# Kernel tuning notes

Hardware: AMD Instinct MI355X
Metric: run time of the kernel (lower is better)

The kernel has to match this reference:

```python
import jax, jax.numpy as jnp
import numpy as np

N_HEAD = 16

def setup_inputs() -> dict:
    key = jax.random.key(0)
    k1, k2, k3 = jax.random.split(key, 3)
    B, T, C = 4, 2048, 2048
    x = jax.random.normal(k1, (B, T, C), dtype=jnp.float32)
    # nn.Linear weights stored as [out, in]; we keep [in, out] for x @ W
    Wqkv = jax.random.normal(k2, (C, 3 * C), dtype=jnp.float32) * (1.0 / np.sqrt(C))
    Wproj = jax.random.normal(k3, (C, C), dtype=jnp.float32) * (1.0 / np.sqrt(C))
    return {"x": x, "Wqkv": Wqkv, "Wproj": Wproj}

def reference(x, Wqkv, Wproj):
    B, T, C = x.shape
    H = N_HEAD
    hd = C // H
    qkv = x @ Wqkv                                  # [B,T,3C]
    qkv = qkv.reshape(B, T, 3, H, hd)
    q = qkv[:, :, 0].transpose(0, 2, 1, 3)          # [B,H,T,hd]
    k = qkv[:, :, 1].transpose(0, 2, 1, 3)
    v = qkv[:, :, 2].transpose(0, 2, 1, 3)
    scale = 1.0 / np.sqrt(hd).astype(np.float32)
    scores = jnp.einsum('bhqd,bhkd->bhqk', q, k) * scale
    causal = jnp.tril(jnp.ones((T, T), dtype=bool))
    scores = jnp.where(causal, scores, jnp.finfo(scores.dtype).min)
    attn = jax.nn.softmax(scores, axis=-1)
    y = jnp.einsum('bhqk,bhkd->bhqd', attn, v)      # [B,H,T,hd]
    y = y.transpose(0, 2, 1, 3).reshape(B, T, C)
    return y @ Wproj  # dropout is identity in eval / p=0
```

## Files before the change

kernel.cpp:

```cpp
#include <hip/hip_runtime.h>
#include <hip/hip_bf16.h>
#include <cstdint>

typedef __bf16 bf16;
typedef __bf16 bf16x8 __attribute__((ext_vector_type(8)));
typedef float f32x4 __attribute__((ext_vector_type(4)));
typedef float f32x8 __attribute__((ext_vector_type(8)));
typedef uint32_t u32x4 __attribute__((ext_vector_type(4)));

constexpr int Bz = 4, T = 2048, Cdim = 2048, NH = 16, HD = 128;
constexpr int QKVC = 3 * Cdim;
constexpr int QKC = 2 * Cdim;
constexpr float NEG_BIG = -3.0e4f;

__device__ __forceinline__ void load_lds16(const bf16* g, const bf16* l) {
  __builtin_amdgcn_global_load_lds(
      (const __attribute__((address_space(1))) void*)g,
      (__attribute__((address_space(3))) void*)l, 16, 0, 0);
}

__device__ __forceinline__ uint32_t pack2bf(float lo, float hi) {
  uint16_t a = __builtin_bit_cast(uint16_t, (bf16)lo);
  uint16_t b = __builtin_bit_cast(uint16_t, (bf16)hi);
  return ((uint32_t)b << 16) | (uint32_t)a;
}

__global__ __launch_bounds__(256)
void cvt_bf16_k(const float* __restrict__ in, bf16* __restrict__ out) {
  size_t i = (size_t)blockIdx.x * 256 + threadIdx.x;
  f32x8 v = *(const f32x8*)(in + i * 8);
  bf16x8 h;
#pragma unroll
  for (int j = 0; j < 8; ++j) h[j] = (bf16)v[j];
  *(bf16x8*)(out + i * 8) = h;
}

__global__ __launch_bounds__(256)
void transpose_cvt_k(const float* __restrict__ in, bf16* __restrict__ out,
                     int R, int Ccols) {
  __shared__ bf16 tile[32][33];
  int c0 = blockIdx.x * 32, r0 = blockIdx.y * 32;
  int tx = threadIdx.x, ty = threadIdx.y;
#pragma unroll
  for (int i = 0; i < 4; ++i)
    tile[ty + i * 8][tx] = (bf16)in[(size_t)(r0 + ty + i * 8) * Ccols + c0 + tx];
  __syncthreads();
#pragma unroll
  for (int i = 0; i < 4; ++i)
    out[(size_t)(c0 + ty + i * 8) * R + r0 + tx] = tile[tx][ty + i * 8];
}

template <bool CF32, bool SCATV>
__global__ __launch_bounds__(512, 2)
void gemm256_k(const bf16* __restrict__ A, const bf16* __restrict__ BT,
               void* __restrict__ Craw, bf16* __restrict__ Vt,
               int M, int N, int K, int ldc) {
  extern __shared__ bf16 lds[];
  const int nK = K >> 6;

  const int nbx = gridDim.x;
  const int nwg = nbx * gridDim.y;
  const int orig = blockIdx.x + blockIdx.y * nbx;
  const int q8 = nwg >> 3;
  const int wgid = (orig & 7) * q8 + (orig >> 3);
  const size_t col0 = (size_t)(wgid % nbx) * 256;
  const size_t row0 = (size_t)(wgid / nbx) * 256;

  const int tid = threadIdx.x;
  const int w = tid >> 6, lane = tid & 63;
  const int qn = lane & 15, quad = lane >> 4;
  const int wm = w >> 2, wn = w & 3;

  const int rl8 = lane >> 3;
  const int scol = ((lane & 7) ^ rl8) << 3;
  const size_t gOff = (size_t)(w * 8 + rl8) * K + scol;
  const int ldsW = w * 512;

  const int csA0 = (quad * 8) ^ ((qn & 7) << 3);
  const int csA1 = (32 + quad * 8) ^ ((qn & 7) << 3);
  const int aBaseIdx = wm * 8192 + qn * 64;
  const int bBaseIdx = 16384 + (wn >> 1) * 8192 + ((wn & 1) * 64 + qn) * 64;

  f32x4 acc[8][4];
  f32x4 zero4 = {0.f, 0.f, 0.f, 0.f};
#pragma unroll
  for (int m = 0; m < 8; ++m)
#pragma unroll
    for (int n = 0; n < 4; ++n) acc[m][n] = zero4;

  auto stageA = [&](int c, int h, int t) {
    const bf16* g = A + (row0 + h * 128) * (size_t)K + (size_t)t * 64 + gOff;
    const bf16* l = lds + c * 32768 + h * 8192 + ldsW;
    load_lds16(g, l);
    load_lds16(g + (size_t)64 * K, l + 4096);
  };
  auto stageB = [&](int c, int h, int t) {
    const bf16* g = BT + (col0 + h * 128) * (size_t)K + (size_t)t * 64 + gOff;
    const bf16* l = lds + c * 32768 + 16384 + h * 8192 + ldsW;
    load_lds16(g, l);
    load_lds16(g + (size_t)64 * K, l + 4096);
  };

  stageA(0, 0, 0); stageA(0, 1, 0);
  stageB(0, 0, 0); stageB(0, 1, 0);
  if (nK > 1) { stageB(1, 0, 1); stageB(1, 1, 1); }
  asm volatile("s_waitcnt vmcnt(4)" ::: "memory");
  asm volatile("s_barrier" ::: "memory");

  for (int t = 0; t < nK; ++t) {
    const int c = t & 1, cn = c ^ 1;
    const int cE = c * 32768;

    bf16x8 a0[4][2], b0[2][2], b1[2][2];
#pragma unroll
    for (int m = 0; m < 4; ++m) {
      a0[m][0] = *(const bf16x8*)&lds[cE + aBaseIdx + m * 1024 + csA0];
      a0[m][1] = *(const bf16x8*)&lds[cE + aBaseIdx + m * 1024 + csA1];
    }
#pragma unroll
    for (int n = 0; n < 2; ++n) {
      b0[n][0] = *(const bf16x8*)&lds[cE + bBaseIdx + n * 1024 + csA0];
      b0[n][1] = *(const bf16x8*)&lds[cE + bBaseIdx + n * 1024 + csA1];
      b1[n][0] = *(const bf16x8*)&lds[cE + bBaseIdx + (n + 2) * 1024 + csA0];
      b1[n][1] = *(const bf16x8*)&lds[cE + bBaseIdx + (n + 2) * 1024 + csA1];
    }
    if (t + 1 < nK) stageA(cn, 1, t + 1);
    __builtin_amdgcn_s_setprio(1);
#pragma unroll
    for (int m = 0; m < 4; ++m)
#pragma unroll
      for (int n = 0; n < 2; ++n) {
        acc[m][n] = __builtin_amdgcn_mfma_f32_16x16x32_bf16(a0[m][0], b0[n][0], acc[m][n], 0, 0, 0);
        acc[m][n] = __builtin_amdgcn_mfma_f32_16x16x32_bf16(a0[m][1], b0[n][1], acc[m][n], 0, 0, 0);
      }
    __builtin_amdgcn_s_setprio(0);
    asm volatile("s_barrier" ::: "memory");

    if (t + 1 < nK) stageA(cn, 0, t + 1);
    __builtin_amdgcn_s_setprio(1);
#pragma unroll
    for (int m = 0; m < 4; ++m)
#pragma unroll
      for (int n = 0; n < 2; ++n) {
        acc[m][n + 2] = __builtin_amdgcn_mfma_f32_16x16x32_bf16(a0[m][0], b1[n][0], acc[m][n + 2], 0, 0, 0);
        acc[m][n + 2] = __builtin_amdgcn_mfma_f32_16x16x32_bf16(a0[m][1], b1[n][1], acc[m][n + 2], 0, 0, 0);
      }
    __builtin_amdgcn_s_setprio(0);
    asm volatile("s_barrier" ::: "memory");

    bf16x8 a1[4][2];
#pragma unroll
    for (int m = 0; m < 4; ++m) {
      a1[m][0] = *(const bf16x8*)&lds[cE + aBaseIdx + (m + 4) * 1024 + csA0];
      a1[m][1] = *(const bf16x8*)&lds[cE + aBaseIdx + (m + 4) * 1024 + csA1];
    }
    if (t + 2 < nK) stageB(c, 0, t + 2);
    __builtin_amdgcn_s_setprio(1);
#pragma unroll
    for (int m = 0; m < 4; ++m)
#pragma unroll
      for (int n = 0; n < 2; ++n) {
        acc[m + 4][n] = __builtin_amdgcn_mfma_f32_16x16x32_bf16(a1[m][0], b0[n][0], acc[m + 4][n], 0, 0, 0);
        acc[m + 4][n] = __builtin_amdgcn_mfma_f32_16x16x32_bf16(a1[m][1], b0[n][1], acc[m + 4][n], 0, 0, 0);
      }
    __builtin_amdgcn_s_setprio(0);
    asm volatile("s_barrier" ::: "memory");

    if (t + 2 < nK) {
      stageB(c, 1, t + 2);
      asm volatile("s_waitcnt vmcnt(4)" ::: "memory");
    } else {
      asm volatile("s_waitcnt vmcnt(0)" ::: "memory");
    }
    __builtin_amdgcn_s_setprio(1);
#pragma unroll
    for (int m = 0; m < 4; ++m)
#pragma unroll
      for (int n = 0; n < 2; ++n) {
        acc[m + 4][n + 2] = __builtin_amdgcn_mfma_f32_16x16x32_bf16(a1[m][0], b1[n][0], acc[m + 4][n + 2], 0, 0, 0);
        acc[m + 4][n + 2] = __builtin_amdgcn_mfma_f32_16x16x32_bf16(a1[m][1], b1[n][1], acc[m + 4][n + 2], 0, 0, 0);
      }
    __builtin_amdgcn_s_setprio(0);
    asm volatile("s_barrier" ::: "memory");
  }

  if (SCATV && (int)col0 >= QKC) {
#pragma unroll
    for (int m = 0; m < 8; ++m)
#pragma unroll
      for (int n = 0; n < 4; ++n)
#pragma unroll
        for (int rr = 0; rr < 4; ++rr) {
          int row = (int)row0 + wm * 128 + m * 16 + quad * 4 + rr;
          int bb = row >> 11, tt = row & (T - 1);
          int cv = (int)col0 + wn * 64 + n * 16 + qn - QKC;
          int hh = cv >> 7, d = cv & 127;
          Vt[((size_t)(bb * NH + hh) * HD + d) * T + tt] = (bf16)acc[m][n][rr];
        }
  } else {
#pragma unroll
    for (int m = 0; m < 8; ++m)
#pragma unroll
      for (int n = 0; n < 4; ++n)
#pragma unroll
        for (int rr = 0; rr < 4; ++rr) {
          size_t idx = (row0 + wm * 128 + m * 16 + quad * 4 + rr) * (size_t)ldc +
                       col0 + wn * 64 + n * 16 + qn;
          if (CF32) ((float*)Craw)[idx] = acc[m][n][rr];
          else      ((bf16*)Craw)[idx] = (bf16)acc[m][n][rr];
        }
  }
}

constexpr int KSTR = 136, VSTR = 72;

__global__ __launch_bounds__(512, 4)
void attn_k(const bf16* __restrict__ qk, const bf16* __restrict__ vt,
            bf16* __restrict__ y) {
  const int b = blockIdx.z, h = blockIdx.y;
  const int qb = (int)(gridDim.x - 1 - blockIdx.x);
  const int qt0 = qb * 128;
  const int tid = threadIdx.x;
  const int w = tid >> 6, lane = tid & 63;
  const int qn = lane & 15, quad = lane >> 4;
  const int q0 = qt0 + w * 16;

  __shared__ __align__(16) bf16 Ks[64 * KSTR];
  __shared__ __align__(16) bf16 Vs[128 * VSTR];

  const bf16* qkB = qk + (size_t)b * T * QKC + h * HD;
  const bf16* vtB = vt + (size_t)(b * NH + h) * HD * T;
  const bf16* kBase = qkB + Cdim;

  bf16x8 qF[4];
  {
    const float scale = 0.088388347648318447f;
    const bf16* qRow = qkB + (size_t)(q0 + qn) * QKC;
#pragma unroll
    for (int c = 0; c < 4; ++c) {
      bf16x8 v = *(const bf16x8*)(qRow + c * 32 + quad * 8);
#pragma unroll
      for (int j = 0; j < 8; ++j) v[j] = (bf16)((float)v[j] * scale);
      qF[c] = v;
    }
  }

  float m_i = NEG_BIG, l_i = 0.f;
  f32x4 zero4 = {0.f, 0.f, 0.f, 0.f};
  f32x4 o[8];
#pragma unroll
  for (int cc = 0; cc < 8; ++cc) o[cc] = zero4;

  const int kr  = tid >> 4;
  const int kc8 = (tid & 15) << 3;
  const int vd  = tid >> 3;
  const int vk8 = (tid & 7) << 3;

  const int addrA = ((lane & 15) + ((quad & 1) << 5)) << 2;
  const int addrB = addrA + 64;

  const int nT = 2 * qb + 2;

  bf16x8 rK0 = *(const bf16x8*)(kBase + (size_t)kr * QKC + kc8);
  bf16x8 rK1 = *(const bf16x8*)(kBase + (size_t)(kr + 32) * QKC + kc8);
  bf16x8 rV0 = *(const bf16x8*)(vtB + (size_t)vd * T + vk8);
  bf16x8 rV1 = *(const bf16x8*)(vtB + (size_t)(vd + 64) * T + vk8);

  for (int t = 0; t < nT; ++t) {
    const int kt0 = t * 64;
    __syncthreads();
    *(bf16x8*)&Ks[kr * KSTR + kc8] = rK0;
    *(bf16x8*)&Ks[(kr + 32) * KSTR + kc8] = rK1;
    *(bf16x8*)&Vs[vd * VSTR + vk8] = rV0;
    *(bf16x8*)&Vs[(vd + 64) * VSTR + vk8] = rV1;
    __syncthreads();
    if (t + 1 < nT) {
      const int kn = kt0 + 64;
      rK0 = *(const bf16x8*)(kBase + (size_t)(kn + kr) * QKC + kc8);
      rK1 = *(const bf16x8*)(kBase + (size_t)(kn + kr + 32) * QKC + kc8);
      rV0 = *(const bf16x8*)(vtB + (size_t)vd * T + kn + vk8);
      rV1 = *(const bf16x8*)(vtB + (size_t)(vd + 64) * T + kn + vk8);
    }
    if (kt0 > q0 + 15) continue;

    f32x4 s[4] = {zero4, zero4, zero4, zero4};
    __builtin_amdgcn_s_setprio(1);
#pragma unroll
    for (int c = 0; c < 4; ++c)
#pragma unroll
      for (int ks = 0; ks < 4; ++ks) {
        bf16x8 kf = *(const bf16x8*)&Ks[(ks * 16 + qn) * KSTR + c * 32 + quad * 8];
        s[ks] = __builtin_amdgcn_mfma_f32_16x16x32_bf16(kf, qF[c], s[ks], 0, 0, 0);
      }
    __builtin_amdgcn_s_setprio(0);

    if (kt0 + 63 > q0) {
      const int qv = q0 + qn;
#pragma unroll
      for (int ks = 0; ks < 4; ++ks)
#pragma unroll
        for (int rr = 0; rr < 4; ++rr)
          if (kt0 + ks * 16 + quad * 4 + rr > qv) s[ks][rr] = NEG_BIG;
    }

    float mx = s[0][0];
#pragma unroll
    for (int ks = 0; ks < 4; ++ks)
#pragma unroll
      for (int rr = 0; rr < 4; ++rr) mx = fmaxf(mx, s[ks][rr]);
    mx = fmaxf(mx, __shfl_xor(mx, 16));
    mx = fmaxf(mx, __shfl_xor(mx, 32));

    if (!__all(mx - m_i <= 8.0f)) {
      float mn = fmaxf(m_i, mx);
      float alpha = __expf(m_i - mn);
      m_i = mn;
      l_i *= alpha;
      float aR[4];
#pragma unroll
      for (int rr = 0; rr < 4; ++rr) aR[rr] = __shfl(alpha, quad * 4 + rr);
#pragma unroll
      for (int cc = 0; cc < 8; ++cc)
#pragma unroll
        for (int rr = 0; rr < 4; ++rr) o[cc][rr] *= aR[rr];
    }

    float rs = 0.f;
#pragma unroll
    for (int ks = 0; ks < 4; ++ks)
#pragma unroll
      for (int rr = 0; rr < 4; ++rr) {
        float pv = __expf(s[ks][rr] - m_i);
        s[ks][rr] = pv;
        rs += pv;
      }
    rs += __shfl_xor(rs, 16);
    rs += __shfl_xor(rs, 32);
    l_i += rs;

    uint32_t pku[4][2];
#pragma unroll
    for (int ks = 0; ks < 4; ++ks)
#pragma unroll
      for (int b2 = 0; b2 < 2; ++b2)
        pku[ks][b2] = pack2bf(s[ks][2 * b2], s[ks][2 * b2 + 1]);

    const int hi2 = quad >> 1;
    __builtin_amdgcn_s_setprio(1);
#pragma unroll
    for (int c = 0; c < 2; ++c) {
      uint32_t lo0A = (uint32_t)__builtin_amdgcn_ds_bpermute(addrA, (int)pku[2 * c][0]);
      uint32_t lo1A = (uint32_t)__builtin_amdgcn_ds_bpermute(addrA, (int)pku[2 * c][1]);
      uint32_t lo0B = (uint32_t)__builtin_amdgcn_ds_bpermute(addrB, (int)pku[2 * c][0]);
      uint32_t lo1B = (uint32_t)__builtin_amdgcn_ds_bpermute(addrB, (int)pku[2 * c][1]);
      uint32_t hi0A = (uint32_t)__builtin_amdgcn_ds_bpermute(addrA, (int)pku[2 * c + 1][0]);
      uint32_t hi1A = (uint32_t)__builtin_amdgcn_ds_bpermute(addrA, (int)pku[2 * c + 1][1]);
      uint32_t hi0B = (uint32_t)__builtin_amdgcn_ds_bpermute(addrB, (int)pku[2 * c + 1][0]);
      uint32_t hi1B = (uint32_t)__builtin_amdgcn_ds_bpermute(addrB, (int)pku[2 * c + 1][1]);
      u32x4 pw;
      pw[0] = hi2 ? hi0A : lo0A;
      pw[1] = hi2 ? hi1A : lo1A;
      pw[2] = hi2 ? hi0B : lo0B;
      pw[3] = hi2 ? hi1B : lo1B;
      bf16x8 pF = __builtin_bit_cast(bf16x8, pw);
#pragma unroll
      for (int cc = 0; cc < 8; ++cc) {
        bf16x8 vf = *(const bf16x8*)&Vs[(cc * 16 + qn) * VSTR + c * 32 + quad * 8];
        o[cc] = __builtin_amdgcn_mfma_f32_16x16x32_bf16(pF, vf, o[cc], 0, 0, 0);
      }
    }
    __builtin_amdgcn_s_setprio(0);
  }

  float linv[4];
#pragma unroll
  for (int rr = 0; rr < 4; ++rr) {
    float lr = __shfl(l_i, quad * 4 + rr);
    linv[rr] = 1.f / fmaxf(lr, 1e-30f);
  }
  bf16* yB = y + (size_t)b * T * Cdim + h * HD;
#pragma unroll
  for (int cc = 0; cc < 8; ++cc)
#pragma unroll
    for (int rr = 0; rr < 4; ++rr)
      yB[(size_t)(q0 + quad * 4 + rr) * Cdim + cc * 16 + qn] =
          (bf16)(o[cc][rr] * linv[rr]);
}

extern "C" void kernel_launch(void* const* d_in, const int* in_sizes, int n_in,
                              void* d_out, int out_size, void* d_ws, size_t ws_size,
                              hipStream_t stream) {
  const float* x     = (const float*)d_in[0];
  const float* Wqkv  = (const float*)d_in[1];
  const float* Wproj = (const float*)d_in[2];
  float* out = (float*)d_out;

  char* ws = (char*)d_ws;
  bf16* qkbuf  = (bf16*)(ws);
  bf16* Vt     = (bf16*)(ws + (size_t)64 * 1024 * 1024);
  bf16* WqkvT  = (bf16*)(ws + (size_t)96 * 1024 * 1024);
  bf16* y      = WqkvT;
  bf16* WprojT = (bf16*)(ws + (size_t)128 * 1024 * 1024);
  bf16* xb     = (bf16*)d_out;

  cvt_bf16_k<<<dim3((Bz * T * Cdim) / (256 * 8)), 256, 0, stream>>>(x, xb);
  transpose_cvt_k<<<dim3(QKVC / 32, Cdim / 32), dim3(32, 8), 0, stream>>>(
      Wqkv, WqkvT, Cdim, QKVC);
  transpose_cvt_k<<<dim3(Cdim / 32, Cdim / 32), dim3(32, 8), 0, stream>>>(
      Wproj, WprojT, Cdim, Cdim);

  gemm256_k<false, true><<<dim3(QKVC / 256, (Bz * T) / 256), 512, 131072, stream>>>(
      xb, WqkvT, (void*)qkbuf, Vt, Bz * T, QKVC, Cdim, QKC);

  attn_k<<<dim3(T / 128, NH, Bz), 512, 0, stream>>>(qkbuf, Vt, y);

  gemm256_k<true, false><<<dim3(Cdim / 256, (Bz * T) / 256), 512, 131072, stream>>>(
      y, WprojT, (void*)out, nullptr, Bz * T, Cdim, Cdim, Cdim);
}
```

Before: 603.8 us.

## Pair complementary causal query tiles per attention block to balance work

Each attention block now handles two 128-row query tiles, qb and 15-qb. The two tiles share every K/V tile loaded into shared memory, and every block gets an equal amount of causal work, which removes the triangular load imbalance and halves the K/V traffic for the short tile. The grid shrinks to half the blocks, and launch bounds drop from 4 to 2 blocks per CU to allow the doubled accumulator and Q registers. Occupancy falls and the per-iteration register pressure rises.

```diff
diff --git a/kernel.cpp b/kernel.cpp
--- a/kernel.cpp
+++ b/kernel.cpp
@@ -214,16 +214,17 @@
 
 constexpr int KSTR = 136, VSTR = 72;
 
-__global__ __launch_bounds__(512, 4)
+__global__ __launch_bounds__(512, 2)
 void attn_k(const bf16* __restrict__ qk, const bf16* __restrict__ vt,
             bf16* __restrict__ y) {
   const int b = blockIdx.z, h = blockIdx.y;
-  const int qb = (int)(gridDim.x - 1 - blockIdx.x);
-  const int qt0 = qb * 128;
+  const int qbA = blockIdx.x;
+  const int qbB = 15 - qbA;
   const int tid = threadIdx.x;
   const int w = tid >> 6, lane = tid & 63;
   const int qn = lane & 15, quad = lane >> 4;
-  const int q0 = qt0 + w * 16;
+  const int q0A = qbA * 128 + w * 16;
+  const int q0B = qbB * 128 + w * 16;
 
   __shared__ __align__(16) bf16 Ks[64 * KSTR];
   __shared__ __align__(16) bf16 Vs[128 * VSTR];
@@ -232,24 +233,29 @@
   const bf16* vtB = vt + (size_t)(b * NH + h) * HD * T;
   const bf16* kBase = qkB + Cdim;
 
-  bf16x8 qF[4];
+  bf16x8 qFA[4], qFB[4];
   {
     const float scale = 0.088388347648318447f;
-    const bf16* qRow = qkB + (size_t)(q0 + qn) * QKC;
+    const bf16* qRowA = qkB + (size_t)(q0A + qn) * QKC;
+    const bf16* qRowB = qkB + (size_t)(q0B + qn) * QKC;
 #pragma unroll
     for (int c = 0; c < 4; ++c) {
-      bf16x8 v = *(const bf16x8*)(qRow + c * 32 + quad * 8);
-#pragma unroll
-      for (int j = 0; j < 8; ++j) v[j] = (bf16)((float)v[j] * scale);
-      qF[c] = v;
-    }
-  }
-
-  float m_i = NEG_BIG, l_i = 0.f;
+      bf16x8 va = *(const bf16x8*)(qRowA + c * 32 + quad * 8);
+      bf16x8 vb = *(const bf16x8*)(qRowB + c * 32 + quad * 8);
+#pragma unroll
+      for (int j = 0; j < 8; ++j) {
+        va[j] = (bf16)((float)va[j] * scale);
+        vb[j] = (bf16)((float)vb[j] * scale);
+      }
+      qFA[c] = va; qFB[c] = vb;
+    }
+  }
+
+  float mA = NEG_BIG, lA = 0.f, mB = NEG_BIG, lB = 0.f;
   f32x4 zero4 = {0.f, 0.f, 0.f, 0.f};
-  f32x4 o[8];
-#pragma unroll
-  for (int cc = 0; cc < 8; ++cc) o[cc] = zero4;
+  f32x4 oA[8], oB[8];
+#pragma unroll
+  for (int cc = 0; cc < 8; ++cc) { oA[cc] = zero4; oB[cc] = zero4; }
 
   const int kr  = tid >> 4;
   const int kc8 = (tid & 15) << 3;
@@ -258,8 +264,75 @@
 
   const int addrA = ((lane & 15) + ((quad & 1) << 5)) << 2;
   const int addrB = addrA + 64;
-
-  const int nT = 2 * qb + 2;
+  const int hi2 = quad >> 1;
+
+  auto softmax_pack = [&](f32x4 (&s)[4], int q0p, int kt0, float& m_i,
+                          float& l_i, f32x4 (&o)[8], uint32_t (&pku)[4][2]) {
+    if (kt0 + 63 > q0p) {
+      const int qv = q0p + qn;
+#pragma unroll
+      for (int ks = 0; ks < 4; ++ks)
+#pragma unroll
+        for (int rr = 0; rr < 4; ++rr)
+          if (kt0 + ks * 16 + quad * 4 + rr > qv) s[ks][rr] = NEG_BIG;
+    }
+    float mx = s[0][0];
+#pragma unroll
+    for (int ks = 0; ks < 4; ++ks)
+#pragma unroll
+      for (int rr = 0; rr < 4; ++rr) mx = fmaxf(mx, s[ks][rr]);
+    mx = fmaxf(mx, __shfl_xor(mx, 16));
+    mx = fmaxf(mx, __shfl_xor(mx, 32));
+    if (!__all(mx - m_i <= 8.0f)) {
+      float mn = fmaxf(m_i, mx);
+      float alpha = __expf(m_i - mn);
+      m_i = mn;
+      l_i *= alpha;
+      float aR[4];
+#pragma unroll
+      for (int rr = 0; rr < 4; ++rr) aR[rr] = __shfl(alpha, quad * 4 + rr);
+#pragma unroll
+      for (int cc = 0; cc < 8; ++cc)
+#pragma unroll
+        for (int rr = 0; rr < 4; ++rr) o[cc][rr] *= aR[rr];
+    }
+    float rs = 0.f;
+#pragma unroll
+    for (int ks = 0; ks < 4; ++ks)
+#pragma unroll
+      for (int rr = 0; rr < 4; ++rr) {
+        float pv = __expf(s[ks][rr] - m_i);
+        s[ks][rr] = pv;
+        rs += pv;
+      }
+    rs += __shfl_xor(rs, 16);
+    rs += __shfl_xor(rs, 32);
+    l_i += rs;
+#pragma unroll
+    for (int ks = 0; ks < 4; ++ks)
+#pragma unroll
+      for (int b2 = 0; b2 < 2; ++b2)
+        pku[ks][b2] = pack2bf(s[ks][2 * b2], s[ks][2 * b2 + 1]);
+  };
+
+  auto redist = [&](uint32_t (&pku)[4][2], int c) -> bf16x8 {
+    uint32_t lo0A = (uint32_t)__builtin_amdgcn_ds_bpermute(addrA, (int)pku[2 * c][0]);
+    uint32_t lo1A = (uint32_t)__builtin_amdgcn_ds_bpermute(addrA, (int)pku[2 * c][1]);
+    uint32_t lo0B = (uint32_t)__builtin_amdgcn_ds_bpermute(addrB, (int)pku[2 * c][0]);
+    uint32_t lo1B = (uint32_t)__builtin_amdgcn_ds_bpermute(addrB, (int)pku[2 * c][1]);
+    uint32_t hi0A = (uint32_t)__builtin_amdgcn_ds_bpermute(addrA, (int)pku[2 * c + 1][0]);
+    uint32_t hi1A = (uint32_t)__builtin_amdgcn_ds_bpermute(addrA, (int)pku[2 * c + 1][1]);
+    uint32_t hi0B = (uint32_t)__builtin_amdgcn_ds_bpermute(addrB, (int)pku[2 * c + 1][0]);
+    uint32_t hi1B = (uint32_t)__builtin_amdgcn_ds_bpermute(addrB, (int)pku[2 * c + 1][1]);
+    u32x4 pw;
+    pw[0] = hi2 ? hi0A : lo0A;
+    pw[1] = hi2 ? hi1A : lo1A;
+    pw[2] = hi2 ? hi0B : lo0B;
+    pw[3] = hi2 ? hi1B : lo1B;
+    return __builtin_bit_cast(bf16x8, pw);
+  };
+
+  const int nT = 2 * qbB + 2;
 
   bf16x8 rK0 = *(const bf16x8*)(kBase + (size_t)kr * QKC + kc8);
   bf16x8 rK1 = *(const bf16x8*)(kBase + (size_t)(kr + 32) * QKC + kc8);
@@ -281,110 +354,93 @@
       rV0 = *(const bf16x8*)(vtB + (size_t)vd * T + kn + vk8);
       rV1 = *(const bf16x8*)(vtB + (size_t)(vd + 64) * T + kn + vk8);
     }
-    if (kt0 > q0 + 15) continue;
-
-    f32x4 s[4] = {zero4, zero4, zero4, zero4};
-    __builtin_amdgcn_s_setprio(1);
-#pragma unroll
-    for (int c = 0; c < 4; ++c)
-#pragma unroll
-      for (int ks = 0; ks < 4; ++ks) {
-        bf16x8 kf = *(const bf16x8*)&Ks[(ks * 16 + qn) * KSTR + c * 32 + quad * 8];
-        s[ks] = __builtin_amdgcn_mfma_f32_16x16x32_bf16(kf, qF[c], s[ks], 0, 0, 0);
-      }
-    __builtin_amdgcn_s_setprio(0);
-
-    if (kt0 + 63 > q0) {
-      const int qv = q0 + qn;
-#pragma unroll
-      for (int ks = 0; ks < 4; ++ks)
-#pragma unroll
-        for (int rr = 0; rr < 4; ++rr)
-          if (kt0 + ks * 16 + quad * 4 + rr > qv) s[ks][rr] = NEG_BIG;
-    }
-
-    float mx = s[0][0];
-#pragma unroll
-    for (int ks = 0; ks < 4; ++ks)
-#pragma unroll
-      for (int rr = 0; rr < 4; ++rr) mx = fmaxf(mx, s[ks][rr]);
-    mx = fmaxf(mx, __shfl_xor(mx, 16));
-    mx = fmaxf(mx, __shfl_xor(mx, 32));
-
-    if (!__all(mx - m_i <= 8.0f)) {
-      float mn = fmaxf(m_i, mx);
-      float alpha = __expf(m_i - mn);
-      m_i = mn;
-      l_i *= alpha;
-      float aR[4];
-#pragma unroll
-      for (int rr = 0; rr < 4; ++rr) aR[rr] = __shfl(alpha, quad * 4 + rr);
-#pragma unroll
-      for (int cc = 0; cc < 8; ++cc)
-#pragma unroll
-        for (int rr = 0; rr < 4; ++rr) o[cc][rr] *= aR[rr];
-    }
-
-    float rs = 0.f;
-#pragma unroll
-    for (int ks = 0; ks < 4; ++ks)
-#pragma unroll
-      for (int rr = 0; rr < 4; ++rr) {
-        float pv = __expf(s[ks][rr] - m_i);
-        s[ks][rr] = pv;
-        rs += pv;
-      }
-    rs += __shfl_xor(rs, 16);
-    rs += __shfl_xor(rs, 32);
-    l_i += rs;
-
-    uint32_t pku[4][2];
-#pragma unroll
-    for (int ks = 0; ks < 4; ++ks)
-#pragma unroll
-      for (int b2 = 0; b2 < 2; ++b2)
-        pku[ks][b2] = pack2bf(s[ks][2 * b2], s[ks][2 * b2 + 1]);
-
-    const int hi2 = quad >> 1;
-    __builtin_amdgcn_s_setprio(1);
-#pragma unroll
-    for (int c = 0; c < 2; ++c) {
-      uint32_t lo0A = (uint32_t)__builtin_amdgcn_ds_bpermute(addrA, (int)pku[2 * c][0]);
-      uint32_t lo1A = (uint32_t)__builtin_amdgcn_ds_bpermute(addrA, (int)pku[2 * c][1]);
-      uint32_t lo0B = (uint32_t)__builtin_amdgcn_ds_bpermute(addrB, (int)pku[2 * c][0]);
-      uint32_t lo1B = (uint32_t)__builtin_amdgcn_ds_bpermute(addrB, (int)pku[2 * c][1]);
-      uint32_t hi0A = (uint32_t)__builtin_amdgcn_ds_bpermute(addrA, (int)pku[2 * c + 1][0]);
-      uint32_t hi1A = (uint32_t)__builtin_amdgcn_ds_bpermute(addrA, (int)pku[2 * c + 1][1]);
-      uint32_t hi0B = (uint32_t)__builtin_amdgcn_ds_bpermute(addrB, (int)pku[2 * c + 1][0]);
-      uint32_t hi1B = (uint32_t)__builtin_amdgcn_ds_bpermute(addrB, (int)pku[2 * c + 1][1]);
-      u32x4 pw;
-      pw[0] = hi2 ? hi0A : lo0A;
-      pw[1] = hi2 ? hi1A : lo1A;
-      pw[2] = hi2 ? hi0B : lo0B;
-      pw[3] = hi2 ? hi1B : lo1B;
-      bf16x8 pF = __builtin_bit_cast(bf16x8, pw);
-#pragma unroll
-      for (int cc = 0; cc < 8; ++cc) {
-        bf16x8 vf = *(const bf16x8*)&Vs[(cc * 16 + qn) * VSTR + c * 32 + quad * 8];
-        o[cc] = __builtin_amdgcn_mfma_f32_16x16x32_bf16(pF, vf, o[cc], 0, 0, 0);
-      }
-    }
-    __builtin_amdgcn_s_setprio(0);
-  }
-
-  float linv[4];
-#pragma unroll
-  for (int rr = 0; rr < 4; ++rr) {
-    float lr = __shfl(l_i, quad * 4 + rr);
-    linv[rr] = 1.f / fmaxf(lr, 1e-30f);
-  }
+    const bool actA = (kt0 <= q0A + 15);
+    const bool actB = (kt0 <= q0B + 15);
+    if (!actB) continue;
+
+    f32x4 sA[4] = {zero4, zero4, zero4, zero4};
+    f32x4 sB[4] = {zero4, zero4, zero4, zero4};
+    __builtin_amdgcn_s_setprio(1);
+    if (actA) {
+#pragma unroll
+      for (int c = 0; c < 4; ++c)
+#pragma unroll
+        for (int ks = 0; ks < 4; ++ks) {
+          bf16x8 kf = *(const bf16x8*)&Ks[(ks * 16 + qn) * KSTR + c * 32 + quad * 8];
+          sA[ks] = __builtin_amdgcn_mfma_f32_16x16x32_bf16(kf, qFA[c], sA[ks], 0, 0, 0);
+          sB[ks] = __builtin_amdgcn_mfma_f32_16x16x32_bf16(kf, qFB[c], sB[ks], 0, 0, 0);
+        }
+    } else {
+#pragma unroll
+      for (int c = 0; c < 4; ++c)
+#pragma unroll
+        for (int ks = 0; ks < 4; ++ks) {
+          bf16x8 kf = *(const bf16x8*)&Ks[(ks * 16 + qn) * KSTR + c * 32 + quad * 8];
+          sB[ks] = __builtin_amdgcn_mfma_f32_16x16x32_bf16(kf, qFB[c], sB[ks], 0, 0, 0);
+        }
+    }
+    __builtin_amdgcn_s_setprio(0);
+
+    uint32_t pkuA[4][2], pkuB[4][2];
+    if (actA) softmax_pack(sA, q0A, kt0, mA, lA, oA, pkuA);
+    softmax_pack(sB, q0B, kt0, mB, lB, oB, pkuB);
+
+    __builtin_amdgcn_s_setprio(1);
+    if (actA) {
+#pragma unroll
+      for (int c = 0; c < 2; ++c) {
+        bf16x8 pFA = redist(pkuA, c);
+        bf16x8 pFB = redist(pkuB, c);
+#pragma unroll
+        for (int cc = 0; cc < 8; ++cc) {
+          bf16x8 vf = *(const bf16x8*)&Vs[(cc * 16 + qn) * VSTR + c * 32 + quad * 8];
+          oA[cc] = __builtin_amdgcn_mfma_f32_16x16x32_bf16(pFA, vf, oA[cc], 0, 0, 0);
+          oB[cc] = __builtin_amdgcn_mfma_f32_16x16x32_bf16(pFB, vf, oB[cc], 0, 0, 0);
+        }
+      }
+    } else {
+#pragma unroll
+      for (int c = 0; c < 2; ++c) {
+        bf16x8 pFB = redist(pkuB, c);
+#pragma unroll
+        for (int cc = 0; cc < 8; ++cc) {
+          bf16x8 vf = *(const bf16x8*)&Vs[(cc * 16 + qn) * VSTR + c * 32 + quad * 8];
+          oB[cc] = __builtin_amdgcn_mfma_f32_16x16x32_bf16(pFB, vf, oB[cc], 0, 0, 0);
+        }
+      }
+    }
+    __builtin_amdgcn_s_setprio(0);
+  }
+
   bf16* yB = y + (size_t)b * T * Cdim + h * HD;
-#pragma unroll
-  for (int cc = 0; cc < 8; ++cc)
-#pragma unroll
-    for (int rr = 0; rr < 4; ++rr)
-      yB[(size_t)(q0 + quad * 4 + rr) * Cdim + cc * 16 + qn] =
-          (bf16)(o[cc][rr] * linv[rr]);
+  {
+    float linv[4];
+#pragma unroll
+    for (int rr = 0; rr < 4; ++rr) {
+      float lr = __shfl(lA, quad * 4 + rr);
+      linv[rr] = 1.f / fmaxf(lr, 1e-30f);
+    }
+#pragma unroll
+    for (int cc = 0; cc < 8; ++cc)
+#pragma unroll
+      for (int rr = 0; rr < 4; ++rr)
+        yB[(size_t)(q0A + quad * 4 + rr) * Cdim + cc * 16 + qn] =
+            (bf16)(oA[cc][rr] * linv[rr]);
+  }
+  {
+    float linv[4];
+#pragma unroll
+    for (int rr = 0; rr < 4; ++rr) {
+      float lr = __shfl(lB, quad * 4 + rr);
+      linv[rr] = 1.f / fmaxf(lr, 1e-30f);
+    }
+#pragma unroll
+    for (int cc = 0; cc < 8; ++cc)
+#pragma unroll
+      for (int rr = 0; rr < 4; ++rr)
+        yB[(size_t)(q0B + quad * 4 + rr) * Cdim + cc * 16 + qn] =
+            (bf16)(oB[cc][rr] * linv[rr]);
+  }
 }
 
 extern "C" void kernel_launch(void* const* d_in, const int* in_sizes, int n_in,
@@ -412,7 +468,7 @@
   gemm256_k<false, true><<<dim3(QKVC / 256, (Bz * T) / 256), 512, 131072, stream>>>(
       xb, WqkvT, (void*)qkbuf, Vt, Bz * T, QKVC, Cdim, QKC);
 
-  attn_k<<<dim3(T / 128, NH, Bz), 512, 0, stream>>>(qkbuf, Vt, y);
+  attn_k<<<dim3(T / 256, NH, Bz), 512, 0, stream>>>(qkbuf, Vt, y);
 
   gemm256_k<true, false><<<dim3(Cdim / 256, (Bz * T) / 256), 512, 131072, stream>>>(
       y, WprojT, (void*)out, nullptr, Bz * T, Cdim, Cdim, Cdim);
```

Result: faster. 550.3 us (-8.9%).
